# Performance work log

Hardware: AMD Instinct MI355X
Metric: run time of the kernel (lower is better)

The kernel has to match this reference:

```python
import jax, jax.numpy as jnp
import numpy as np

B, K, D = 8, 256, 256   # batch, num_nodes (== node_embedding_dim), embed dim
ALPHA = 0.2             # LeakyReLU negative slope


def setup_inputs() -> dict:
    key = jax.random.key(0)
    ks = jax.random.split(key, 6)
    x = jax.random.normal(ks[0], (B, K, D), jnp.float32)
    adj = jax.random.randint(ks[1], (B, K, K), 0, 2).astype(jnp.int32)
    # lin: Linear(2*D, D)  -> weight (D, 2D), bias (D,)
    W = jax.random.normal(ks[2], (D, 2 * D), jnp.float32) * (1.0 / np.sqrt(2 * D))
    b_lin = jax.random.normal(ks[3], (D,), jnp.float32) * 0.02
    # attention vector a: (D, 1) in torch; use (D,) here
    a = jax.random.normal(ks[4], (D,), jnp.float32) * (1.414 / np.sqrt(D))
    # per-pair bias (num_nodes, num_nodes); zeros-init in torch, small randn for grad testing
    bias = jax.random.normal(ks[5], (K, K), jnp.float32) * 0.01
    return {"x": x, "adj": adj, "W": W, "b_lin": b_lin, "a": a, "bias": bias}


def reference(x, adj, W, b_lin, a, bias):
    # x: (B, K, D) -> transpose to (B, D, K); with K == D the 'nodes' axis is axis 1.
    v = jnp.swapaxes(x, 1, 2)                      # (B, N, F) with N = D, F = K
    residual = v                                   # residual_proj is Identity (use_gatv2)
    # GATv2: lin([v_i || v_j]) = W1 @ v_i + W2 @ v_j + b  (split W along input dim)
    W1, W2 = W[:, :K], W[:, K:]                    # each (D, K)
    left = jnp.einsum('bnf,df->bnd', v, W1)        # (B, N, D)
    right = jnp.einsum('bnf,df->bnd', v, W2)       # (B, N, D)
    pre = left[:, :, None, :] + right[:, None, :, :] + b_lin   # (B, N, N, D)
    h = jnp.where(pre > 0, pre, ALPHA * pre)       # LeakyReLU
    e = jnp.einsum('bijd,d->bij', h, a)            # (B, N, N)
    e = e + bias                                   # use_bias
    neg_inf = jnp.float32(-jnp.inf)
    e = jnp.where(adj == 0, neg_inf, e)            # masked_fill
    all_inf = jnp.all(e == neg_inf, axis=2, keepdims=True)
    e = jnp.where(all_inf, jnp.float32(0.0), e)    # rows fully masked -> uniform attn
    attn = jax.nn.softmax(e, axis=2)               # dropout inactive (eval / p=0)
    out = jax.nn.sigmoid(attn @ v) + residual      # (B, N, F)
    return jnp.swapaxes(out, 1, 2)                 # back to (B, K, D)
```

## Files before the change

kernel.cpp:

```cpp
#include <hip/hip_runtime.h>
#include <hip/hip_bf16.h>
#include <math.h>

#define BB 8
#define BS 65536

typedef __attribute__((ext_vector_type(8))) short short8v;
typedef __attribute__((ext_vector_type(4))) float f32x4;
typedef unsigned short u16;
typedef __attribute__((address_space(1))) const void gv_t;
typedef __attribute__((address_space(3))) void lv_t;

__device__ __forceinline__ u16 f2bf(float v) {
  __hip_bfloat16 h = __float2bfloat16(v);
  return *reinterpret_cast<u16*>(&h);
}

__device__ __forceinline__ short8v frag(const u16* lds, int rb, int sk,
                                        int lane) {
  int r = rb * 16 + (lane & 15);
  int c = sk * 4 + (lane >> 4);
  int cs = c ^ (r & 7);
  return *(const short8v*)(lds + r * 64 + cs * 8);
}

__device__ __forceinline__ void stage_g32(const u16* __restrict__ g, int row0,
                                          int stride, int k0, u16* lds,
                                          int tid) {
  int r = tid >> 3, c = tid & 7;
  int cs = c ^ (r & 7);
  const u16* src = g + (size_t)(row0 + r) * stride + k0 + cs * 8;
  u16* dst = lds + (size_t)(tid & ~63) * 8;
  __builtin_amdgcn_global_load_lds((gv_t*)src, (lv_t*)dst, 16, 0, 0);
}

__global__ __launch_bounds__(256) void d1_proj(
    const float* __restrict__ x, const float* __restrict__ W,
    const float* __restrict__ b_lin, const float* __restrict__ a,
    float* __restrict__ L2p, float* __restrict__ R2t) {
  __shared__ float xf[64][33];
  __shared__ u16 XT[32 * 64], B1[32 * 64], B2[32 * 64];
  const int bk = blockIdx.x, tid = threadIdx.x;
  const int b = bk & 7, t = bk >> 3;
  const int n0 = (t >> 3) * 32, dd0 = (t & 7) * 32;
  const int lane = tid & 63, wid = tid >> 6;
  const int nh = wid >> 1, dh = wid & 1;
  const float* xb = x + (size_t)b * BS;

  const int r8 = tid >> 5, c32 = tid & 31;
  const int rw = tid >> 3, cw = tid & 7;

  f32x4 accL = f32x4{0.f, 0.f, 0.f, 0.f};
  f32x4 accR = f32x4{0.f, 0.f, 0.f, 0.f};

  for (int ks = 0; ks < 4; ++ks) {
    float xr[8];
#pragma unroll
    for (int it = 0; it < 8; ++it)
      xr[it] = xb[(size_t)(ks * 64 + it * 8 + r8) * 256 + n0 + c32];
    float4 wa0 = *(const float4*)&W[(size_t)(dd0 + rw) * 512 + ks * 64 + cw * 8];
    float4 wa1 = *(const float4*)&W[(size_t)(dd0 + rw) * 512 + ks * 64 + cw * 8 + 4];
    float4 wb0 = *(const float4*)&W[(size_t)(dd0 + rw) * 512 + 256 + ks * 64 + cw * 8];
    float4 wb1 = *(const float4*)&W[(size_t)(dd0 + rw) * 512 + 256 + ks * 64 + cw * 8 + 4];
#pragma unroll
    for (int it = 0; it < 8; ++it) xf[it * 8 + r8][c32] = xr[it];
    __syncthreads();
    {
      u16 o[8];
#pragma unroll
      for (int e = 0; e < 8; ++e) o[e] = f2bf(xf[cw * 8 + e][rw]);
      *(short8v*)&XT[rw * 64 + ((cw ^ (rw & 7)) * 8)] = *(const short8v*)o;
      u16 o1[8] = {f2bf(wa0.x), f2bf(wa0.y), f2bf(wa0.z), f2bf(wa0.w),
                   f2bf(wa1.x), f2bf(wa1.y), f2bf(wa1.z), f2bf(wa1.w)};
      *(short8v*)&B1[rw * 64 + ((cw ^ (rw & 7)) * 8)] = *(const short8v*)o1;
      u16 o2[8] = {f2bf(wb0.x), f2bf(wb0.y), f2bf(wb0.z), f2bf(wb0.w),
                   f2bf(wb1.x), f2bf(wb1.y), f2bf(wb1.z), f2bf(wb1.w)};
      *(short8v*)&B2[rw * 64 + ((cw ^ (rw & 7)) * 8)] = *(const short8v*)o2;
    }
    __syncthreads();
#pragma unroll
    for (int sk = 0; sk < 2; ++sk) {
      short8v xa = frag(XT, nh, sk, lane);
      short8v w1 = frag(B1, dh, sk, lane);
      short8v w2 = frag(B2, dh, sk, lane);
      accL = __builtin_amdgcn_mfma_f32_16x16x32_bf16(xa, w1, accL, 0, 0, 0);
      accR = __builtin_amdgcn_mfma_f32_16x16x32_bf16(w2, xa, accR, 0, 0, 0);
    }
  }

  {
    int ddc = dd0 + dh * 16 + (lane & 15);
    float c2 = fabsf(0.4f * a[ddc]);
    float bl = b_lin[ddc];
    int nr = n0 + nh * 16 + ((lane >> 4) << 2);
#pragma unroll
    for (int q = 0; q < 4; ++q)
      L2p[(size_t)b * BS + (size_t)(nr + q) * 256 + ddc] = c2 * (accL[q] + bl);
  }
  {
    int nc = n0 + nh * 16 + (lane & 15);
    int ddr = dd0 + dh * 16 + ((lane >> 4) << 2);
#pragma unroll
    for (int q = 0; q < 4; ++q) {
      float c2 = fabsf(0.4f * a[ddr + q]);
      R2t[(size_t)b * BS + (size_t)(ddr + q) * 256 + nc] = c2 * accR[q];
    }
  }
}

__global__ __launch_bounds__(512) void d2_scores(
    const float* __restrict__ R2t, const float* __restrict__ L2p,
    const float* __restrict__ a, const int* __restrict__ adj,
    const float* __restrict__ bias, u16* __restrict__ attnh) {
  __shared__ float4 Lq[2][256];
  __shared__ float sS[256];
  __shared__ float redm[8][4], reds[8][4];
  const int t = threadIdx.x, j = t & 255, ih = t >> 8;
  const int bk = blockIdx.x, b = bk & 7, i0 = (bk >> 3) * 8;
  {
    const float* Lb = L2p + (size_t)b * BS + (size_t)(i0 + ih * 4) * 256;
    Lq[ih][j] = make_float4(Lb[j], Lb[256 + j], Lb[512 + j], Lb[768 + j]);
    if (t < 256) sS[t] = (a[t] >= 0.f) ? 1.f : -1.f;
  }
  __syncthreads();

  const float* Rb = R2t + (size_t)b * BS;
  float e0 = 0.f, e1 = 0.f, e2 = 0.f, e3 = 0.f, srj = 0.f;
#pragma unroll 16
  for (int d = 0; d < 256; ++d) {
    float rv = Rb[d * 256 + j];
    float4 lq = Lq[ih][d];
    float sd = sS[d];
    srj = fmaf(sd, rv, srj);
    float t0 = lq.x + rv, t1 = lq.y + rv, t2 = lq.z + rv, t3 = lq.w + rv;
    e0 = fmaf(sd, fabsf(t0), e0);
    e1 = fmaf(sd, fabsf(t1), e1);
    e2 = fmaf(sd, fabsf(t2), e2);
    e3 = fmaf(sd, fabsf(t3), e3);
  }
  float ev[4] = {e0, e1, e2, e3};
  const float sbase = 1.5f * srj;
  const float NEG_INF = -__builtin_inff();
#pragma unroll
  for (int ii = 0; ii < 4; ++ii) {
    int row = i0 + ih * 4 + ii;
    ev[ii] += sbase + bias[row * 256 + j];
    ev[ii] = (adj[(size_t)b * BS + (size_t)row * 256 + j] == 0) ? NEG_INF
                                                                : ev[ii];
  }
  const int wid = t >> 6, lane = t & 63, wb = ih * 4;
#pragma unroll
  for (int ii = 0; ii < 4; ++ii) {
    float v = ev[ii];
#pragma unroll
    for (int off = 32; off >= 1; off >>= 1) v = fmaxf(v, __shfl_xor(v, off, 64));
    if (lane == 0) redm[wid][ii] = v;
  }
  __syncthreads();
  float p4[4];
#pragma unroll
  for (int ii = 0; ii < 4; ++ii) {
    float m = fmaxf(fmaxf(redm[wb][ii], redm[wb + 1][ii]),
                    fmaxf(redm[wb + 2][ii], redm[wb + 3][ii]));
    p4[ii] = (m == NEG_INF) ? 1.f : __expf(ev[ii] - m);
  }
#pragma unroll
  for (int ii = 0; ii < 4; ++ii) {
    float v = p4[ii];
#pragma unroll
    for (int off = 32; off >= 1; off >>= 1) v += __shfl_xor(v, off, 64);
    if (lane == 0) reds[wid][ii] = v;
  }
  __syncthreads();
#pragma unroll
  for (int ii = 0; ii < 4; ++ii) {
    float ssum = reds[wb][ii] + reds[wb + 1][ii] + reds[wb + 2][ii] +
                 reds[wb + 3][ii];
    attnh[(size_t)b * BS + (size_t)(i0 + ih * 4 + ii) * 256 + j] =
        f2bf(p4[ii] / ssum);
  }
}

__global__ __launch_bounds__(256) void d3_out(const u16* __restrict__ attnh,
                                              const float* __restrict__ x,
                                              float* __restrict__ out) {
  __shared__ u16 At[32 * 64], Bt[32 * 64];
  const int bk = blockIdx.x, tid = threadIdx.x;
  const int b = bk & 7, t = bk >> 3;
  const int f0 = (t >> 3) * 32, i0 = (t & 7) * 32;
  const int lane = tid & 63, wid = tid >> 6;
  const int fh = wid >> 1, ih2 = wid & 1;
  const float* Ax = x + (size_t)b * BS;
  const u16* Bb = attnh + (size_t)b * BS;
  const int rw = tid >> 3, cw = tid & 7;

  f32x4 acc = f32x4{0.f, 0.f, 0.f, 0.f};
  for (int ks = 0; ks < 4; ++ks) {
    stage_g32(Bb, i0, 256, ks * 64, Bt, tid);
    {
      const float* src = Ax + (size_t)(f0 + rw) * 256 + ks * 64 + cw * 8;
      float4 v0 = *(const float4*)src;
      float4 v1 = *(const float4*)(src + 4);
      u16 o[8] = {f2bf(v0.x), f2bf(v0.y), f2bf(v0.z), f2bf(v0.w),
                  f2bf(v1.x), f2bf(v1.y), f2bf(v1.z), f2bf(v1.w)};
      *(short8v*)&At[rw * 64 + ((cw ^ (rw & 7)) * 8)] = *(const short8v*)o;
    }
    __syncthreads();
#pragma unroll
    for (int sk = 0; sk < 2; ++sk) {
      short8v af = frag(At, fh, sk, lane);
      short8v bf = frag(Bt, ih2, sk, lane);
      acc = __builtin_amdgcn_mfma_f32_16x16x32_bf16(af, bf, acc, 0, 0, 0);
    }
    __syncthreads();
  }

  int col = i0 + ih2 * 16 + (lane & 15);
  int rbase = f0 + fh * 16 + ((lane >> 4) << 2);
#pragma unroll
  for (int q = 0; q < 4; ++q) {
    size_t idx = (size_t)b * BS + (size_t)(rbase + q) * 256 + col;
    float sg = 1.f / (1.f + __expf(-acc[q]));
    out[idx] = sg + x[idx];
  }
}

extern "C" void kernel_launch(void* const* d_in, const int* in_sizes, int n_in,
                              void* d_out, int out_size, void* d_ws,
                              size_t ws_size, hipStream_t stream) {
  const float* x = (const float*)d_in[0];
  const int* adj = (const int*)d_in[1];
  const float* W = (const float*)d_in[2];
  const float* b_lin = (const float*)d_in[3];
  const float* a = (const float*)d_in[4];
  const float* bias = (const float*)d_in[5];
  float* out = (float*)d_out;

  float* L2p = (float*)d_ws;
  float* R2t = L2p + BB * BS;
  u16* attnh = (u16*)(R2t + BB * BS);

  d1_proj<<<512, 256, 0, stream>>>(x, W, b_lin, a, L2p, R2t);
  d2_scores<<<256, 512, 0, stream>>>(R2t, L2p, a, adj, bias, attnh);
  d3_out<<<512, 256, 0, stream>>>(attnh, x, out);
}
```

Measured before the change: 28.68 us.

## Store right projection as packed bf16 and double-buffer it into LDS

The right-projection buffer is written in bf16, packed two per 32-bit word, which halves its size. The score kernel now streams it into LDS with async global_load_lds in double-buffered 16-row slices, and it loads adj and bias before the main loop so their latency overlaps the compute. This aims to cut global memory traffic and load latency in the score kernel, which reads the whole buffer once per block. The cost is lower precision in the score sums and extra barriers per slice.

Result: slower. 31.06 us (+8.3%).

```diff
diff --git a/kernel.cpp b/kernel.cpp
--- a/kernel.cpp
+++ b/kernel.cpp
@@ -8,6 +8,7 @@
 typedef __attribute__((ext_vector_type(8))) short short8v;
 typedef __attribute__((ext_vector_type(4))) float f32x4;
 typedef unsigned short u16;
+typedef unsigned int u32;
 typedef __attribute__((address_space(1))) const void gv_t;
 typedef __attribute__((address_space(3))) void lv_t;
 
@@ -37,7 +38,7 @@
 __global__ __launch_bounds__(256) void d1_proj(
     const float* __restrict__ x, const float* __restrict__ W,
     const float* __restrict__ b_lin, const float* __restrict__ a,
-    float* __restrict__ L2p, float* __restrict__ R2t) {
+    float* __restrict__ L2p, u32* __restrict__ R2p) {
   __shared__ float xf[64][33];
   __shared__ u16 XT[32 * 64], B1[32 * 64], B2[32 * 64];
   const int bk = blockIdx.x, tid = threadIdx.x;
@@ -100,23 +101,46 @@
   {
     int nc = n0 + nh * 16 + (lane & 15);
     int ddr = dd0 + dh * 16 + ((lane >> 4) << 2);
-#pragma unroll
-    for (int q = 0; q < 4; ++q) {
-      float c2 = fabsf(0.4f * a[ddr + q]);
-      R2t[(size_t)b * BS + (size_t)(ddr + q) * 256 + nc] = c2 * accR[q];
-    }
+    float r0 = fabsf(0.4f * a[ddr + 0]) * accR[0];
+    float r1 = fabsf(0.4f * a[ddr + 1]) * accR[1];
+    float r2 = fabsf(0.4f * a[ddr + 2]) * accR[2];
+    float r3 = fabsf(0.4f * a[ddr + 3]) * accR[3];
+    u32 p01 = (u32)f2bf(r0) | ((u32)f2bf(r1) << 16);
+    u32 p23 = (u32)f2bf(r2) | ((u32)f2bf(r3) << 16);
+    u32* Rp = R2p + (size_t)b * 32768;
+    Rp[(size_t)(ddr >> 1) * 256 + nc] = p01;
+    Rp[(size_t)((ddr >> 1) + 1) * 256 + nc] = p23;
   }
 }
 
 __global__ __launch_bounds__(512) void d2_scores(
-    const float* __restrict__ R2t, const float* __restrict__ L2p,
+    const u32* __restrict__ R2p, const float* __restrict__ L2p,
     const float* __restrict__ a, const int* __restrict__ adj,
     const float* __restrict__ bias, u16* __restrict__ attnh) {
+  __shared__ u32 Rs[2][16 * 256];
   __shared__ float4 Lq[2][256];
   __shared__ float sS[256];
   __shared__ float redm[8][4], reds[8][4];
   const int t = threadIdx.x, j = t & 255, ih = t >> 8;
   const int bk = blockIdx.x, b = bk & 7, i0 = (bk >> 3) * 8;
+  const u32* Rb = R2p + (size_t)b * 32768;
+
+  {
+    const u32* src = Rb + t * 4;
+    u32* dst = &Rs[0][0] + (size_t)(t & ~63) * 4;
+    __builtin_amdgcn_global_load_lds((gv_t*)src, (lv_t*)dst, 16, 0, 0);
+    src = Rb + 2048 + t * 4;
+    dst = &Rs[0][2048] + (size_t)(t & ~63) * 4;
+    __builtin_amdgcn_global_load_lds((gv_t*)src, (lv_t*)dst, 16, 0, 0);
+  }
+  int adjv[4];
+  float biasv[4];
+#pragma unroll
+  for (int ii = 0; ii < 4; ++ii) {
+    int row = i0 + ih * 4 + ii;
+    adjv[ii] = adj[(size_t)b * BS + (size_t)row * 256 + j];
+    biasv[ii] = bias[row * 256 + j];
+  }
   {
     const float* Lb = L2p + (size_t)b * BS + (size_t)(i0 + ih * 4) * 256;
     Lq[ih][j] = make_float4(Lb[j], Lb[256 + j], Lb[512 + j], Lb[768 + j]);
@@ -124,29 +148,47 @@
   }
   __syncthreads();
 
-  const float* Rb = R2t + (size_t)b * BS;
   float e0 = 0.f, e1 = 0.f, e2 = 0.f, e3 = 0.f, srj = 0.f;
-#pragma unroll 16
-  for (int d = 0; d < 256; ++d) {
-    float rv = Rb[d * 256 + j];
-    float4 lq = Lq[ih][d];
-    float sd = sS[d];
-    srj = fmaf(sd, rv, srj);
-    float t0 = lq.x + rv, t1 = lq.y + rv, t2 = lq.z + rv, t3 = lq.w + rv;
-    e0 = fmaf(sd, fabsf(t0), e0);
-    e1 = fmaf(sd, fabsf(t1), e1);
-    e2 = fmaf(sd, fabsf(t2), e2);
-    e3 = fmaf(sd, fabsf(t3), e3);
-  }
+  for (int s = 0; s < 8; ++s) {
+    if (s < 7) {
+      const u32* src = Rb + (s + 1) * 4096 + t * 4;
+      u32* dst = &Rs[(s + 1) & 1][0] + (size_t)(t & ~63) * 4;
+      __builtin_amdgcn_global_load_lds((gv_t*)src, (lv_t*)dst, 16, 0, 0);
+      src += 2048;
+      dst = &Rs[(s + 1) & 1][2048] + (size_t)(t & ~63) * 4;
+      __builtin_amdgcn_global_load_lds((gv_t*)src, (lv_t*)dst, 16, 0, 0);
+    }
+    const u32* Rslice = &Rs[s & 1][0];
+    const int d2base = s * 16;
+#pragma unroll 8
+    for (int q = 0; q < 16; ++q) {
+      int d2 = d2base + q;
+      u32 u = Rslice[q * 256 + j];
+      float rv0 = __uint_as_float(u << 16);
+      float rv1 = __uint_as_float(u & 0xffff0000u);
+      float s0 = sS[2 * d2], s1 = sS[2 * d2 + 1];
+      float4 lq0 = Lq[ih][2 * d2], lq1 = Lq[ih][2 * d2 + 1];
+      srj = fmaf(s0, rv0, srj);
+      srj = fmaf(s1, rv1, srj);
+      e0 = fmaf(s0, fabsf(lq0.x + rv0), e0);
+      e1 = fmaf(s0, fabsf(lq0.y + rv0), e1);
+      e2 = fmaf(s0, fabsf(lq0.z + rv0), e2);
+      e3 = fmaf(s0, fabsf(lq0.w + rv0), e3);
+      e0 = fmaf(s1, fabsf(lq1.x + rv1), e0);
+      e1 = fmaf(s1, fabsf(lq1.y + rv1), e1);
+      e2 = fmaf(s1, fabsf(lq1.z + rv1), e2);
+      e3 = fmaf(s1, fabsf(lq1.w + rv1), e3);
+    }
+    if (s < 7) __syncthreads();
+  }
+
   float ev[4] = {e0, e1, e2, e3};
   const float sbase = 1.5f * srj;
   const float NEG_INF = -__builtin_inff();
 #pragma unroll
   for (int ii = 0; ii < 4; ++ii) {
-    int row = i0 + ih * 4 + ii;
-    ev[ii] += sbase + bias[row * 256 + j];
-    ev[ii] = (adj[(size_t)b * BS + (size_t)row * 256 + j] == 0) ? NEG_INF
-                                                                : ev[ii];
+    ev[ii] += sbase + biasv[ii];
+    ev[ii] = (adjv[ii] == 0) ? NEG_INF : ev[ii];
   }
   const int wid = t >> 6, lane = t & 63, wb = ih * 4;
 #pragma unroll
@@ -237,10 +279,10 @@
   float* out = (float*)d_out;
 
   float* L2p = (float*)d_ws;
-  float* R2t = L2p + BB * BS;
-  u16* attnh = (u16*)(R2t + BB * BS);
-
-  d1_proj<<<512, 256, 0, stream>>>(x, W, b_lin, a, L2p, R2t);
-  d2_scores<<<256, 512, 0, stream>>>(R2t, L2p, a, adj, bias, attnh);
+  u32* R2p = (u32*)(L2p + BB * BS);
+  u16* attnh = (u16*)(R2p + BB * 32768);
+
+  d1_proj<<<512, 256, 0, stream>>>(x, W, b_lin, a, L2p, R2p);
+  d2_scores<<<256, 512, 0, stream>>>(R2p, L2p, a, adj, bias, attnh);
   d3_out<<<512, 256, 0, stream>>>(attnh, x, out);
 }
```
